# Kernel tuning notes

Hardware: AMD Instinct MI355X
Metric: run time of the kernel (lower is better)

Reference implementation:

```python
import jax, jax.numpy as jnp
import numpy as np

SMOOTH = 1.0
EPS = 1e-8
K_SKEL = 50  # soft_skel default; module's self.k is unused in forward


def _max_pool3d(x, w):
    # x: (b, c, D, H, W); w: 3-tuple window; stride 1, 'same'-style padding (k-1)//2
    window = (1, 1) + tuple(w)
    pad = [(0, 0), (0, 0)] + [((k - 1) // 2, (k - 1) // 2) for k in w]
    return jax.lax.reduce_window(x, -jnp.inf, jax.lax.max, window, (1,) * 5, pad)


def soft_erode(I):
    p1 = -_max_pool3d(-I, (3, 1, 1))
    p2 = -_max_pool3d(-I, (1, 3, 1))
    p3 = -_max_pool3d(-I, (1, 1, 3))
    return jnp.minimum(jnp.minimum(p1, p3), p2)


def soft_dilate(I):
    return _max_pool3d(I, (3, 3, 3))


def soft_open(I):
    return soft_dilate(soft_erode(I))


def soft_skel(img, k=K_SKEL):
    skel = jax.nn.relu(img - soft_open(img))

    @jax.checkpoint
    def body(carry, _):
        img, skel = carry
        img = soft_erode(img)
        delta = jax.nn.relu(img - soft_open(img))
        skel = skel + jax.nn.relu(delta - skel * delta)
        return (img, skel), None

    (_, skel), _ = jax.lax.scan(body, (img, skel), None, length=k)
    return skel


def setup_inputs() -> dict:
    key = jax.random.key(0)
    kx, ky = jax.random.split(key)
    shape = (2, 2, 80, 80, 80)
    x = jax.random.uniform(kx, shape, dtype=jnp.float32)
    y = jax.random.uniform(ky, shape, dtype=jnp.float32)
    return {"x": x, "y": y}


def reference(x, y):
    # batch_dice=False -> reduce over spatial axes only
    axes = (2, 3, 4)
    clp = soft_skel(x)
    cll = soft_skel(y)
    # shapes equal -> y_onehot is the soft target itself
    tp = jnp.sum(x * cll, axis=axes)             # (b, c)
    fn = jnp.sum((1.0 - x) * cll, axis=axes)
    tpc = jnp.sum(clp * y, axis=axes)
    fpc = jnp.sum(clp * (1.0 - y), axis=axes)
    clp2voll = (tpc + SMOOTH) / (tpc + fpc + SMOOTH)
    cll2volp = (tp + SMOOTH) / (tp + fn + SMOOTH)
    dc = 2.0 * clp2voll * cll2volp / (cll2volp + clp2voll + EPS)
    return 1.0 - dc.mean()  # do_bg=True -> no channel slicing
```

## Files before the change

### kernel.cpp

```cpp
#include <hip/hip_runtime.h>

#define DDIM 80
#define PLANE 6400
#define VOL 512000
#define HALFV 4
#define NVOL 8
#define NTOT (NVOL*VOL)
#define NCH 20
#define RP 84
#define BLK 256

#define PTY 8
#define PCZ 10
#define PE1R 12
#define PHR 10
#define PNYT 10
#define PNZC 8
#define PGRID (NVOL*PNYT*PNZC)

#define STY 10
#define SCZ 5
#define SNYT 8
#define SNZC 16
#define SER (STY + 2)
#define SGRID (NVOL*SNYT*SNZC)

__device__ __forceinline__ float4 f4min(float4 a, float4 b) {
    return make_float4(fminf(a.x,b.x), fminf(a.y,b.y), fminf(a.z,b.z), fminf(a.w,b.w));
}
__device__ __forceinline__ float4 f4max(float4 a, float4 b) {
    return make_float4(fmaxf(a.x,b.x), fmaxf(a.y,b.y), fmaxf(a.z,b.z), fmaxf(a.w,b.w));
}
__device__ __forceinline__ int s4(int v){ return (v + 8) & 3; }
__device__ __forceinline__ int s2(int v){ return (v + 8) & 1; }
__device__ __forceinline__ float updf(float s, float d){ return s + fmaxf(d - s*d, 0.0f); }

__device__ __forceinline__ void lbar() {
    asm volatile("s_waitcnt lgkmcnt(0)\n\ts_barrier" ::: "memory");
}

struct EIn { float4 c, zA, zB, yA, yB; float lf, rt; };

template<bool FIRST>
__global__ __launch_bounds__(BLK, 3) void pair_k(const float* __restrict__ xin,
                                                 const float* __restrict__ yin,
                                                 const float* __restrict__ a,
                                                 float* __restrict__ eout,
                                                 float* __restrict__ skel)
{
    __shared__ float E1[4][PE1R][RP];
    __shared__ float H1[4][PHR][RP];
    __shared__ float E2[2][PHR][RP];
    __shared__ float H2[4][PHR][RP];

    const int b = blockIdx.x;
    const int v   = b / (PNYT*PNZC);
    const int rem = b - v*(PNYT*PNZC);
    const int yt  = rem / PNZC;
    const int zci = rem - yt*PNZC;
    const int y0 = yt*PTY;
    const int z0 = zci*PCZ;

    const float* __restrict__ src =
        FIRST ? ((v < HALFV) ? (xin + v*VOL) : (yin + (v-HALFV)*VOL)) : (a + v*VOL);
    float* __restrict__ ev  = eout + v*VOL;
    float* __restrict__ skv = skel + v*VOL;

    const int tid = threadIdx.x;
    const int r = tid / NCH;
    const int c = tid - r*NCH;
    const int x4 = 4*c;

    auto loadE1 = [&](int zs, EIn& e) {
        if (r < PE1R) {
            const int gy  = y0 - 2 + r;
            const int gyc = min(max(gy, 0), DDIM-1);
            const int zcl = min(max(zs, 0), DDIM-1);
            const int zm = max(zcl-1, 0), zp = min(zcl+1, DDIM-1);
            const int ym = max(gyc-1, 0), yp = min(gyc+1, DDIM-1);
            const float* rc = src + zcl*PLANE + gyc*DDIM;
            e.c  = *(const float4*)(rc + x4);
            e.lf = rc[max(x4-1, 0)];
            e.rt = rc[min(x4+4, DDIM-1)];
            e.zA = *(const float4*)(src + zm*PLANE + gyc*DDIM + x4);
            e.zB = *(const float4*)(src + zp*PLANE + gyc*DDIM + x4);
            e.yA = *(const float4*)(src + zcl*PLANE + ym*DDIM + x4);
            e.yB = *(const float4*)(src + zcl*PLANE + yp*DDIM + x4);
        }
    };

    auto erodeC = [&](const EIn& e) -> float4 {
        float4 m;
        m.x = fminf(fminf(e.lf,  e.c.x), e.c.y);
        m.y = fminf(fminf(e.c.x, e.c.y), e.c.z);
        m.z = fminf(fminf(e.c.y, e.c.z), e.c.w);
        m.w = fminf(fminf(e.c.z, e.c.w), e.rt);
        return f4min(m, f4min(f4min(e.zA, e.zB), f4min(e.yA, e.yB)));
    };

    auto storeE1 = [&](int zs, float4 m) {
        if (r < PE1R) *(float4*)&E1[s4(zs)][r][x4] = m;
    };

    auto hmax1 = [&](int zs) {
        if (r < PHR) {
            const float* row = &E1[s4(zs)][r+1][0];
            const float4 f = *(const float4*)(row + x4);
            const float lf = (c>0)  ? row[x4-1] : f.x;
            const float rt = (c<19) ? row[x4+4] : f.w;
            float4 h;
            h.x = fmaxf(fmaxf(lf,  f.x), f.y);
            h.y = fmaxf(fmaxf(f.x, f.y), f.z);
            h.z = fmaxf(fmaxf(f.y, f.z), f.w);
            h.w = fmaxf(fmaxf(f.z, f.w), rt);
            *(float4*)&H1[s4(zs)][r][x4] = h;
        }
    };

    auto erode2 = [&](int zs, bool gw) {
        if (r < PHR) {
            const float* rc = &E1[s4(zs)][r+1][0];
            const float4 cc = *(const float4*)(rc + x4);
            const float lf = (c>0)  ? rc[x4-1] : cc.x;
            const float rt = (c<19) ? rc[x4+4] : cc.w;
            float4 m;
            m.x = fminf(fminf(lf,   cc.x), cc.y);
            m.y = fminf(fminf(cc.x, cc.y), cc.z);
            m.z = fminf(fminf(cc.y, cc.z), cc.w);
            m.w = fminf(fminf(cc.z, cc.w), rt);
            m = f4min(m, *(const float4*)&E1[s4(zs)][r][x4]);
            m = f4min(m, *(const float4*)&E1[s4(zs)][r+2][x4]);
            m = f4min(m, *(const float4*)&E1[s4(zs-1)][r+1][x4]);
            m = f4min(m, *(const float4*)&E1[s4(zs+1)][r+1][x4]);
            *(float4*)&E2[s2(zs)][r][x4] = m;
            if (gw && r >= 1 && r <= PTY)
                *(float4*)(ev + zs*PLANE + (y0-1+r)*DDIM + x4) = m;
        }
    };

    auto hmax2 = [&](int zs) {
        if (r < PHR) {
            const float* row = &E2[s2(zs)][r][0];
            const float4 f = *(const float4*)(row + x4);
            const float lf = (c>0)  ? row[x4-1] : f.x;
            const float rt = (c<19) ? row[x4+4] : f.w;
            float4 h;
            h.x = fmaxf(fmaxf(lf,  f.x), f.y);
            h.y = fmaxf(fmaxf(f.x, f.y), f.z);
            h.z = fmaxf(fmaxf(f.y, f.z), f.w);
            h.w = fmaxf(fmaxf(f.z, f.w), rt);
            *(float4*)&H2[s4(zs)][r][x4] = h;
        }
    };

    auto loadD1 = [&](int z, float4& img, float4& sk) {
        if (r < PTY) {
            const int off = z*PLANE + (y0 + r)*DDIM + x4;
            img = *(const float4*)(src + off);
            if constexpr (!FIRST) sk = *(const float4*)(skv + off);
        }
    };

    EIn eS0, eS1;
    float4 img2N = make_float4(0,0,0,0), img2P = make_float4(0,0,0,0);
    float4 skA = make_float4(0,0,0,0), skB = skA, skC = skA;
    float4 dImg = skA, dSk = skA;

    loadE1(z0-2, eS0);
    loadE1(z0-1, eS1);
    storeE1(z0-2, erodeC(eS0));
    storeE1(z0-1, erodeC(eS1));
    loadE1(z0,   eS0);
    loadE1(z0+1, eS1);
    lbar();
    storeE1(z0,   erodeC(eS0));
    storeE1(z0+1, erodeC(eS1));
    hmax1(z0-1);
    loadE1(z0+2, eS1);
    lbar();
    hmax1(z0);
    erode2(z0-1, false);
    loadE1(z0+3, eS0);
    lbar();

#pragma unroll
    for (int S = -1; S <= PCZ; ++S) {
        const int z = z0 + S;
        if (S <= PCZ-2) {
            const float4 m = erodeC((S & 1) ? eS1 : eS0);
            storeE1(z+3, m);
        }
        if (S <= PCZ-4) loadE1(z+5, (S & 1) ? eS1 : eS0);
        if (S <= PCZ-2) hmax1(z+2);
        if (S <= PCZ-1) erode2(z+1, S <= PCZ-2);
        hmax2(z);
        if (S >= 0 && S <= PCZ-1) {
            if (r < PTY) img2N = *(const float4*)&E1[s4(z)][r+2][x4];
        }
        if (S <= PCZ-2) loadD1(z+1, dImg, dSk);
        lbar();
        if (S <= PCZ-2) {
            if (r < PTY) {
                float4 dm = make_float4(-1e30f, -1e30f, -1e30f, -1e30f);
#pragma unroll
                for (int s = 0; s < 3; ++s)
#pragma unroll
                    for (int l = 0; l < 3; ++l)
                        dm = f4max(dm, *(const float4*)&H1[s4(z+s)][r + l][x4]);
                float4 dl;
                dl.x = fmaxf(dImg.x - dm.x, 0.0f);
                dl.y = fmaxf(dImg.y - dm.y, 0.0f);
                dl.z = fmaxf(dImg.z - dm.z, 0.0f);
                dl.w = fmaxf(dImg.w - dm.w, 0.0f);
                if constexpr (FIRST) {
                    skC = dl;
                } else {
                    skC.x = updf(dSk.x, dl.x); skC.y = updf(dSk.y, dl.y);
                    skC.z = updf(dSk.z, dl.z); skC.w = updf(dSk.w, dl.w);
                }
            }
        }
        if (S >= 1) {
            if (r < PTY) {
                float4 dm = make_float4(-1e30f, -1e30f, -1e30f, -1e30f);
#pragma unroll
                for (int s = 0; s < 3; ++s)
#pragma unroll
                    for (int l = 0; l < 3; ++l)
                        dm = f4max(dm, *(const float4*)&H2[s4(z-2+s)][r + l][x4]);
                float4 dl;
                dl.x = fmaxf(img2P.x - dm.x, 0.0f);
                dl.y = fmaxf(img2P.y - dm.y, 0.0f);
                dl.z = fmaxf(img2P.z - dm.z, 0.0f);
                dl.w = fmaxf(img2P.w - dm.w, 0.0f);
                float4 sf;
                sf.x = updf(skA.x, dl.x); sf.y = updf(skA.y, dl.y);
                sf.z = updf(skA.z, dl.z); sf.w = updf(skA.w, dl.w);
                *(float4*)(skv + (z-1)*PLANE + (y0 + r)*DDIM + x4) = sf;
            }
        }
        skA = skB; skB = skC;
        img2P = img2N;
    }
}

template<bool FIRST, bool LASTK>
__global__ __launch_bounds__(BLK, 4) void iter_k(const float* __restrict__ xin,
                                                 const float* __restrict__ yin,
                                                 const float* __restrict__ a,
                                                 float* __restrict__ eout,
                                                 float* __restrict__ skel)
{
    __shared__ float E[3][SER][RP];
    __shared__ float H[4][SER][RP];

    const int b = blockIdx.x;
    const int v   = b >> 7;
    const int rem = b & 127;
    const int yt  = rem >> 4;
    const int zci = rem & 15;
    const int y0 = yt*STY;
    const int z0 = zci*SCZ;

    const float* __restrict__ src =
        FIRST ? ((v < HALFV) ? (xin + v*VOL) : (yin + (v-HALFV)*VOL)) : (a + v*VOL);
    float* __restrict__ ev = LASTK ? nullptr : (eout + v*VOL);
    float* __restrict__ skv = skel + v*VOL;

    const int tid = threadIdx.x;
    const int r = tid / NCH;
    const int c = tid - r*NCH;
    const int x4 = 4*c;

    auto slotE = [](int vv){ return (vv + 9) % 3; };

    auto loadE = [&](int zs, EIn& e) {
        if (tid < SER*NCH) {
            const int gy  = y0 - 1 + r;
            const int gyc = min(max(gy, 0), DDIM-1);
            const int zcl = min(max(zs, 0), DDIM-1);
            const int zm = max(zcl-1, 0), zp = min(zcl+1, DDIM-1);
            const int ym = max(gyc-1, 0), yp = min(gyc+1, DDIM-1);
            const float* rc = src + zcl*PLANE + gyc*DDIM;
            e.c  = *(const float4*)(rc + x4);
            e.lf = rc[max(x4-1, 0)];
            e.rt = rc[min(x4+4, DDIM-1)];
            e.zA = *(const float4*)(src + zm*PLANE + gyc*DDIM + x4);
            e.zB = *(const float4*)(src + zp*PLANE + gyc*DDIM + x4);
            e.yA = *(const float4*)(src + zcl*PLANE + ym*DDIM + x4);
            e.yB = *(const float4*)(src + zcl*PLANE + yp*DDIM + x4);
        }
    };
    auto erodeC = [&](const EIn& e) -> float4 {
        float4 m;
        m.x = fminf(fminf(e.lf,  e.c.x), e.c.y);
        m.y = fminf(fminf(e.c.x, e.c.y), e.c.z);
        m.z = fminf(fminf(e.c.y, e.c.z), e.c.w);
        m.w = fminf(fminf(e.c.z, e.c.w), e.rt);
        return f4min(m, f4min(f4min(e.zA, e.zB), f4min(e.yA, e.yB)));
    };
    auto storeE = [&](int zs, const float4& m) {
        if (tid < SER*NCH) {
            *(float4*)&E[slotE(zs)][r][x4] = m;
            if constexpr (!LASTK) {
                if (r >= 1 && r <= STY && zs >= z0 && zs < z0 + SCZ)
                    *(float4*)(ev + zs*PLANE + (y0 + r - 1)*DDIM + x4) = m;
            }
        }
    };
    auto hmaxStore = [&](int zs, const float4& m) {
        if (tid < SER*NCH) {
            const float* er = &E[slotE(zs)][r][0];
            const float lf = (c > 0)  ? er[x4-1] : m.x;
            const float rt = (c < 19) ? er[x4+4] : m.w;
            float4 h;
            h.x = fmaxf(fmaxf(lf,  m.x), m.y);
            h.y = fmaxf(fmaxf(m.x, m.y), m.z);
            h.z = fmaxf(fmaxf(m.y, m.z), m.w);
            h.w = fmaxf(fmaxf(m.z, m.w), rt);
            *(float4*)&H[s4(zs)][r][x4] = h;
        }
    };
    auto loadD = [&](int z, float4& img, float4& sk) {
        if (tid < STY*NCH) {
            const int off = z*PLANE + (y0 + r)*DDIM + x4;
            img = *(const float4*)(src + off);
            if constexpr (!FIRST) sk = *(const float4*)(skv + off);
        }
    };
    auto dilateUpd = [&](int z, const float4& img, const float4& skin) {
        if (tid < STY*NCH) {
            float4 dm = make_float4(-1e30f, -1e30f, -1e30f, -1e30f);
#pragma unroll
            for (int s = 0; s < 3; ++s)
#pragma unroll
                for (int l = 0; l < 3; ++l)
                    dm = f4max(dm, *(const float4*)&H[s4(z-1+s)][r + l][x4]);
            float4 dl;
            dl.x = fmaxf(img.x - dm.x, 0.0f);
            dl.y = fmaxf(img.y - dm.y, 0.0f);
            dl.z = fmaxf(img.z - dm.z, 0.0f);
            dl.w = fmaxf(img.w - dm.w, 0.0f);
            float4 s;
            if constexpr (FIRST) { s = dl; }
            else {
                s = skin;
                s.x = updf(s.x, dl.x); s.y = updf(s.y, dl.y);
                s.z = updf(s.z, dl.z); s.w = updf(s.w, dl.w);
            }
            *(float4*)(skv + z*PLANE + (y0 + r)*DDIM + x4) = s;
        }
    };

    EIn eP, eQ, eR;
    float4 m0, m1, m2, mPrev, mNew;
    float4 dImg, dSk, dImgN, dSkN;

    loadE(z0-1, eP);
    loadE(z0,   eQ);
    loadE(z0+1, eR);
    m0 = erodeC(eP);  storeE(z0-1, m0);
    m1 = erodeC(eQ);  storeE(z0,   m1);
    lbar();
    loadE(z0+2, eP);
    loadE(z0+3, eQ);
    hmaxStore(z0-1, m0);
    hmaxStore(z0,   m1);
    m2 = erodeC(eR);  storeE(z0+1, m2);
    loadD(z0, dImg, dSk);
    lbar();
    mPrev = m2;

#pragma unroll
    for (int S = 0; S < SCZ; ++S) {
        const int z = z0 + S;
        if (S <= SCZ-2) {
            mNew = erodeC((S & 1) ? eQ : eP);
            storeE(z+2, mNew);
        }
        if (S <= SCZ-4) loadE(z+4, (S & 1) ? eQ : eP);
        hmaxStore(z+1, mPrev);
        if (S <= SCZ-2) loadD(z+1, dImgN, dSkN);
        lbar();
        dilateUpd(z, dImg, dSk);
        if (S <= SCZ-2) { mPrev = mNew; dImg = dImgN; dSk = dSkN; }
    }
}

__global__ __launch_bounds__(256) void reduce_k(const float* __restrict__ x,
                                                const float* __restrict__ y,
                                                const float* __restrict__ skel,
                                                float* __restrict__ partials) {
    const int blk = blockIdx.x;
    const int v = blk >> 8;
    const int sub = blk & 255;
    const int base4 = (v * VOL + sub * 2000) >> 2;
    const float4* x4 = (const float4*)x;
    const float4* y4 = (const float4*)y;
    const float4* clp4 = (const float4*)(skel);
    const float4* cll4 = (const float4*)(skel + HALFV * VOL);
    float s1 = 0, s2 = 0, s3 = 0, s4_ = 0;
    for (int j = threadIdx.x; j < 500; j += 256) {
        const int i4 = base4 + j;
        const float4 xv = x4[i4];
        const float4 yv = y4[i4];
        const float4 cp = clp4[i4];
        const float4 cl = cll4[i4];
        s1 += xv.x*cl.x + xv.y*cl.y + xv.z*cl.z + xv.w*cl.w;
        s2 += cl.x + cl.y + cl.z + cl.w;
        s3 += cp.x*yv.x + cp.y*yv.y + cp.z*yv.z + cp.w*yv.w;
        s4_ += cp.x + cp.y + cp.z + cp.w;
    }
    for (int off = 32; off > 0; off >>= 1) {
        s1 += __shfl_down(s1, off);
        s2 += __shfl_down(s2, off);
        s3 += __shfl_down(s3, off);
        s4_ += __shfl_down(s4_, off);
    }
    __shared__ float smm[4][4];
    const int wave = threadIdx.x >> 6;
    if ((threadIdx.x & 63) == 0) {
        smm[wave][0] = s1; smm[wave][1] = s2; smm[wave][2] = s3; smm[wave][3] = s4_;
    }
    __syncthreads();
    if (threadIdx.x == 0) {
        float a0 = 0, a1 = 0, a2 = 0, a3 = 0;
        for (int w = 0; w < 4; ++w) { a0 += smm[w][0]; a1 += smm[w][1]; a2 += smm[w][2]; a3 += smm[w][3]; }
        partials[blk*4 + 0] = a0;
        partials[blk*4 + 1] = a1;
        partials[blk*4 + 2] = a2;
        partials[blk*4 + 3] = a3;
    }
}

__global__ void final_k(const float* __restrict__ p, float* __restrict__ out) {
    __shared__ float sums[16];
    const int t = threadIdx.x;
    if (t < 16) {
        const int v = t >> 2, k = t & 3;
        float acc = 0.0f;
        for (int b = 0; b < 256; ++b) acc += p[((v << 8) + b)*4 + k];
        sums[t] = acc;
    }
    __syncthreads();
    if (t == 0) {
        float acc = 0.0f;
        for (int v = 0; v < 4; ++v) {
            const float tp      = sums[v*4 + 0];
            const float sum_cll = sums[v*4 + 1];
            const float tpc     = sums[v*4 + 2];
            const float sum_clp = sums[v*4 + 3];
            const float fn  = sum_cll - tp;
            const float fpc = sum_clp - tpc;
            const float clp2voll = (tpc + 1.0f) / (tpc + fpc + 1.0f);
            const float cll2volp = (tp + 1.0f) / (tp + fn + 1.0f);
            acc += 2.0f * clp2voll * cll2volp / (cll2volp + clp2voll + 1e-8f);
        }
        out[0] = 1.0f - acc * 0.25f;
    }
}

extern "C" void kernel_launch(void* const* d_in, const int* in_sizes, int n_in,
                              void* d_out, int out_size, void* d_ws, size_t ws_size,
                              hipStream_t stream) {
    const float* x = (const float*)d_in[0];
    const float* y = (const float*)d_in[1];
    float* out = (float*)d_out;

    float* bufA = (float*)d_ws;
    float* bufB = bufA + NTOT;
    float* skel = bufB + NTOT;
    float* partials = skel + NTOT;

    pair_k<true><<<PGRID, BLK, 0, stream>>>(x, y, nullptr, bufA, skel);
    for (int j = 1; j <= 24; ++j) {
        float* srcb = (j & 1) ? bufA : bufB;
        float* dstb = (j & 1) ? bufB : bufA;
        pair_k<false><<<PGRID, BLK, 0, stream>>>(nullptr, nullptr, srcb, dstb, skel);
    }
    iter_k<false, true><<<SGRID, BLK, 0, stream>>>(nullptr, nullptr, bufA, nullptr, skel);

    reduce_k<<<1024, 256, 0, stream>>>(x, y, skel, partials);
    final_k<<<1, 64, 0, stream>>>(partials, out);
}
```

Baseline: 724.5 us.

## Fuse final skeleton iteration with Dice reduction and enlarge pair-kernel tiles

The last iteration kernel now computes the skeleton update and accumulates the dot-product and sum partials directly. This removes the skeleton write-back and the separate reduction kernel that re-read x, y and both skeletons. The pair kernel's tile grows from 8 to 10 rows, with 320-thread blocks and a 512-block grid, which cuts halo redundancy at the cost of more shared memory and lower occupancy. The final kernel is remapped to the new partial layout.

```diff
diff --git a/kernel.cpp b/kernel.cpp
--- a/kernel.cpp
+++ b/kernel.cpp
@@ -8,22 +8,19 @@
 #define NTOT (NVOL*VOL)
 #define NCH 20
 #define RP 84
-#define BLK 256
-
-#define PTY 8
+
+#define PTY 10
 #define PCZ 10
-#define PE1R 12
-#define PHR 10
-#define PNYT 10
-#define PNZC 8
-#define PGRID (NVOL*PNYT*PNZC)
+#define PE1R 14
+#define PHR 12
+#define PBLK 320
+#define PGRID 512
 
 #define STY 10
 #define SCZ 5
-#define SNYT 8
-#define SNZC 16
 #define SER (STY + 2)
-#define SGRID (NVOL*SNYT*SNZC)
+#define SBLK 256
+#define SGRID 1024
 
 __device__ __forceinline__ float4 f4min(float4 a, float4 b) {
     return make_float4(fminf(a.x,b.x), fminf(a.y,b.y), fminf(a.z,b.z), fminf(a.w,b.w));
@@ -42,11 +39,11 @@
 struct EIn { float4 c, zA, zB, yA, yB; float lf, rt; };
 
 template<bool FIRST>
-__global__ __launch_bounds__(BLK, 3) void pair_k(const float* __restrict__ xin,
-                                                 const float* __restrict__ yin,
-                                                 const float* __restrict__ a,
-                                                 float* __restrict__ eout,
-                                                 float* __restrict__ skel)
+__global__ __launch_bounds__(PBLK, 2) void pair_k(const float* __restrict__ xin,
+                                                  const float* __restrict__ yin,
+                                                  const float* __restrict__ a,
+                                                  float* __restrict__ eout,
+                                                  float* __restrict__ skel)
 {
     __shared__ float E1[4][PE1R][RP];
     __shared__ float H1[4][PHR][RP];
@@ -54,10 +51,10 @@
     __shared__ float H2[4][PHR][RP];
 
     const int b = blockIdx.x;
-    const int v   = b / (PNYT*PNZC);
-    const int rem = b - v*(PNYT*PNZC);
-    const int yt  = rem / PNZC;
-    const int zci = rem - yt*PNZC;
+    const int v   = b >> 6;
+    const int rem = b & 63;
+    const int yt  = rem >> 3;
+    const int zci = rem & 7;
     const int y0 = yt*PTY;
     const int z0 = zci*PCZ;
 
@@ -244,15 +241,15 @@
     }
 }
 
-template<bool FIRST, bool LASTK>
-__global__ __launch_bounds__(BLK, 4) void iter_k(const float* __restrict__ xin,
-                                                 const float* __restrict__ yin,
-                                                 const float* __restrict__ a,
-                                                 float* __restrict__ eout,
-                                                 float* __restrict__ skel)
+__global__ __launch_bounds__(SBLK, 4) void last_k(const float* __restrict__ xin,
+                                                  const float* __restrict__ yin,
+                                                  const float* __restrict__ a,
+                                                  float* __restrict__ skel,
+                                                  float* __restrict__ partials)
 {
     __shared__ float E[3][SER][RP];
     __shared__ float H[4][SER][RP];
+    __shared__ float smm[4][2];
 
     const int b = blockIdx.x;
     const int v   = b >> 7;
@@ -262,10 +259,10 @@
     const int y0 = yt*STY;
     const int z0 = zci*SCZ;
 
-    const float* __restrict__ src =
-        FIRST ? ((v < HALFV) ? (xin + v*VOL) : (yin + (v-HALFV)*VOL)) : (a + v*VOL);
-    float* __restrict__ ev = LASTK ? nullptr : (eout + v*VOL);
-    float* __restrict__ skv = skel + v*VOL;
+    const float* __restrict__ src = a + v*VOL;
+    const float* __restrict__ skv = skel + v*VOL;
+    const float* __restrict__ cnt =
+        (v < HALFV) ? (yin + v*VOL) : (xin + (v-HALFV)*VOL);
 
     const int tid = threadIdx.x;
     const int r = tid / NCH;
@@ -300,13 +297,7 @@
         return f4min(m, f4min(f4min(e.zA, e.zB), f4min(e.yA, e.yB)));
     };
     auto storeE = [&](int zs, const float4& m) {
-        if (tid < SER*NCH) {
-            *(float4*)&E[slotE(zs)][r][x4] = m;
-            if constexpr (!LASTK) {
-                if (r >= 1 && r <= STY && zs >= z0 && zs < z0 + SCZ)
-                    *(float4*)(ev + zs*PLANE + (y0 + r - 1)*DDIM + x4) = m;
-            }
-        }
+        if (tid < SER*NCH) *(float4*)&E[slotE(zs)][r][x4] = m;
     };
     auto hmaxStore = [&](int zs, const float4& m) {
         if (tid < SER*NCH) {
@@ -321,14 +312,18 @@
             *(float4*)&H[s4(zs)][r][x4] = h;
         }
     };
-    auto loadD = [&](int z, float4& img, float4& sk) {
+    auto loadD = [&](int z, float4& img, float4& sk, float4& cv) {
         if (tid < STY*NCH) {
             const int off = z*PLANE + (y0 + r)*DDIM + x4;
             img = *(const float4*)(src + off);
-            if constexpr (!FIRST) sk = *(const float4*)(skv + off);
-        }
-    };
-    auto dilateUpd = [&](int z, const float4& img, const float4& skin) {
+            sk  = *(const float4*)(skv + off);
+            cv  = *(const float4*)(cnt + off);
+        }
+    };
+
+    float sa = 0.0f, sb = 0.0f;
+
+    auto dilateUpd = [&](int z, const float4& img, const float4& skin, const float4& cv) {
         if (tid < STY*NCH) {
             float4 dm = make_float4(-1e30f, -1e30f, -1e30f, -1e30f);
 #pragma unroll
@@ -342,19 +337,16 @@
             dl.z = fmaxf(img.z - dm.z, 0.0f);
             dl.w = fmaxf(img.w - dm.w, 0.0f);
             float4 s;
-            if constexpr (FIRST) { s = dl; }
-            else {
-                s = skin;
-                s.x = updf(s.x, dl.x); s.y = updf(s.y, dl.y);
-                s.z = updf(s.z, dl.z); s.w = updf(s.w, dl.w);
-            }
-            *(float4*)(skv + z*PLANE + (y0 + r)*DDIM + x4) = s;
+            s.x = updf(skin.x, dl.x); s.y = updf(skin.y, dl.y);
+            s.z = updf(skin.z, dl.z); s.w = updf(skin.w, dl.w);
+            sa += cv.x*s.x + cv.y*s.y + cv.z*s.z + cv.w*s.w;
+            sb += s.x + s.y + s.z + s.w;
         }
     };
 
     EIn eP, eQ, eR;
     float4 m0, m1, m2, mPrev, mNew;
-    float4 dImg, dSk, dImgN, dSkN;
+    float4 dImg, dSk, dCv, dImgN, dSkN, dCvN;
 
     loadE(z0-1, eP);
     loadE(z0,   eQ);
@@ -367,7 +359,7 @@
     hmaxStore(z0-1, m0);
     hmaxStore(z0,   m1);
     m2 = erodeC(eR);  storeE(z0+1, m2);
-    loadD(z0, dImg, dSk);
+    loadD(z0, dImg, dSk, dCv);
     lbar();
     mPrev = m2;
 
@@ -380,56 +372,24 @@
         }
         if (S <= SCZ-4) loadE(z+4, (S & 1) ? eQ : eP);
         hmaxStore(z+1, mPrev);
-        if (S <= SCZ-2) loadD(z+1, dImgN, dSkN);
+        if (S <= SCZ-2) loadD(z+1, dImgN, dSkN, dCvN);
         lbar();
-        dilateUpd(z, dImg, dSk);
-        if (S <= SCZ-2) { mPrev = mNew; dImg = dImgN; dSk = dSkN; }
-    }
-}
-
-__global__ __launch_bounds__(256) void reduce_k(const float* __restrict__ x,
-                                                const float* __restrict__ y,
-                                                const float* __restrict__ skel,
-                                                float* __restrict__ partials) {
-    const int blk = blockIdx.x;
-    const int v = blk >> 8;
-    const int sub = blk & 255;
-    const int base4 = (v * VOL + sub * 2000) >> 2;
-    const float4* x4 = (const float4*)x;
-    const float4* y4 = (const float4*)y;
-    const float4* clp4 = (const float4*)(skel);
-    const float4* cll4 = (const float4*)(skel + HALFV * VOL);
-    float s1 = 0, s2 = 0, s3 = 0, s4_ = 0;
-    for (int j = threadIdx.x; j < 500; j += 256) {
-        const int i4 = base4 + j;
-        const float4 xv = x4[i4];
-        const float4 yv = y4[i4];
-        const float4 cp = clp4[i4];
-        const float4 cl = cll4[i4];
-        s1 += xv.x*cl.x + xv.y*cl.y + xv.z*cl.z + xv.w*cl.w;
-        s2 += cl.x + cl.y + cl.z + cl.w;
-        s3 += cp.x*yv.x + cp.y*yv.y + cp.z*yv.z + cp.w*yv.w;
-        s4_ += cp.x + cp.y + cp.z + cp.w;
-    }
+        dilateUpd(z, dImg, dSk, dCv);
+        if (S <= SCZ-2) { mPrev = mNew; dImg = dImgN; dSk = dSkN; dCv = dCvN; }
+    }
+
     for (int off = 32; off > 0; off >>= 1) {
-        s1 += __shfl_down(s1, off);
-        s2 += __shfl_down(s2, off);
-        s3 += __shfl_down(s3, off);
-        s4_ += __shfl_down(s4_, off);
-    }
-    __shared__ float smm[4][4];
-    const int wave = threadIdx.x >> 6;
-    if ((threadIdx.x & 63) == 0) {
-        smm[wave][0] = s1; smm[wave][1] = s2; smm[wave][2] = s3; smm[wave][3] = s4_;
-    }
+        sa += __shfl_down(sa, off);
+        sb += __shfl_down(sb, off);
+    }
+    const int wave = tid >> 6;
+    if ((tid & 63) == 0) { smm[wave][0] = sa; smm[wave][1] = sb; }
     __syncthreads();
-    if (threadIdx.x == 0) {
-        float a0 = 0, a1 = 0, a2 = 0, a3 = 0;
-        for (int w = 0; w < 4; ++w) { a0 += smm[w][0]; a1 += smm[w][1]; a2 += smm[w][2]; a3 += smm[w][3]; }
-        partials[blk*4 + 0] = a0;
-        partials[blk*4 + 1] = a1;
-        partials[blk*4 + 2] = a2;
-        partials[blk*4 + 3] = a3;
+    if (tid == 0) {
+        float a0 = 0, a1 = 0;
+        for (int w = 0; w < 4; ++w) { a0 += smm[w][0]; a1 += smm[w][1]; }
+        partials[b*2 + 0] = a0;
+        partials[b*2 + 1] = a1;
     }
 }
 
@@ -437,19 +397,19 @@
     __shared__ float sums[16];
     const int t = threadIdx.x;
     if (t < 16) {
-        const int v = t >> 2, k = t & 3;
+        const int vv = t >> 1, k = t & 1;
         float acc = 0.0f;
-        for (int b = 0; b < 256; ++b) acc += p[((v << 8) + b)*4 + k];
+        for (int j = 0; j < 128; ++j) acc += p[(vv*128 + j)*2 + k];
         sums[t] = acc;
     }
     __syncthreads();
     if (t == 0) {
         float acc = 0.0f;
-        for (int v = 0; v < 4; ++v) {
-            const float tp      = sums[v*4 + 0];
-            const float sum_cll = sums[v*4 + 1];
-            const float tpc     = sums[v*4 + 2];
-            const float sum_clp = sums[v*4 + 3];
+        for (int ch = 0; ch < 4; ++ch) {
+            const float tpc     = sums[ch*2 + 0];
+            const float sum_clp = sums[ch*2 + 1];
+            const float tp      = sums[(4+ch)*2 + 0];
+            const float sum_cll = sums[(4+ch)*2 + 1];
             const float fn  = sum_cll - tp;
             const float fpc = sum_clp - tpc;
             const float clp2voll = (tpc + 1.0f) / (tpc + fpc + 1.0f);
@@ -472,14 +432,12 @@
     float* skel = bufB + NTOT;
     float* partials = skel + NTOT;
 
-    pair_k<true><<<PGRID, BLK, 0, stream>>>(x, y, nullptr, bufA, skel);
+    pair_k<true><<<PGRID, PBLK, 0, stream>>>(x, y, nullptr, bufA, skel);
     for (int j = 1; j <= 24; ++j) {
         float* srcb = (j & 1) ? bufA : bufB;
         float* dstb = (j & 1) ? bufB : bufA;
-        pair_k<false><<<PGRID, BLK, 0, stream>>>(nullptr, nullptr, srcb, dstb, skel);
-    }
-    iter_k<false, true><<<SGRID, BLK, 0, stream>>>(nullptr, nullptr, bufA, nullptr, skel);
-
-    reduce_k<<<1024, 256, 0, stream>>>(x, y, skel, partials);
+        pair_k<false><<<PGRID, PBLK, 0, stream>>>(nullptr, nullptr, srcb, dstb, skel);
+    }
+    last_k<<<SGRID, SBLK, 0, stream>>>(x, y, bufA, skel, partials);
     final_k<<<1, 64, 0, stream>>>(partials, out);
 }
```

Result: slower. 957.2 us (+32.1%).
